# Performance work log

Measured on AMD Instinct MI355X. Metric: run time of the kernel, lower is better.

## Reference

```python
import jax, jax.numpy as jnp
import numpy as np

N, E, B = 8000, 24000, 256
ATOM, BOND, H, HEADS, L = 133, 14, 256, 8, 5
NEG, EPS = 0.2, 1e-5


def _ln(x, g, b):
    m = x.mean(-1, keepdims=True)
    v = ((x - m) ** 2).mean(-1, keepdims=True)
    return (x - m) * jax.lax.rsqrt(v + EPS) * g + b


def setup_inputs() -> dict:
    key = jax.random.key(0)
    ks = jax.random.split(key, 12)
    s = lambda k, shp, fan: (jax.random.normal(k, shp, jnp.float32) / np.float32(np.sqrt(fan)))
    inp = {
        "x": jax.random.normal(ks[0], (N, ATOM), jnp.float32),
        "edge_attr": jax.random.normal(ks[1], (E, BOND), jnp.float32),
        "emb_W": s(ks[2], (ATOM, H), ATOM), "emb_b": jnp.zeros((H,), jnp.float32),
        "emb_g": jnp.ones((H,), jnp.float32), "emb_beta": jnp.zeros((H,), jnp.float32),
        "Wl": s(ks[3], (L, H, HEADS * H), H), "Wr": s(ks[4], (L, H, HEADS * H), H),
        "We": s(ks[5], (L, BOND, HEADS * H), BOND),
        "att": s(ks[6], (L, HEADS, H), H),
        "bias": jnp.zeros((L, H), jnp.float32),
        "ln_g": jnp.ones((L, H), jnp.float32), "ln_b": jnp.zeros((L, H), jnp.float32),
        "g1W": s(ks[7], (H, H // 2), H), "g1b": jnp.zeros((H // 2,), jnp.float32),
        "g2W": s(ks[8], (H // 2, 1), H // 2), "g2b": jnp.zeros((1,), jnp.float32),
        "edge_index": jax.random.randint(ks[9], (2, E), 0, N, dtype=jnp.int32),
        "batch_vec": jnp.sort(jax.random.randint(ks[10], (N,), 0, B, dtype=jnp.int32)),
    }
    return inp


def reference(x, edge_attr, emb_W, emb_b, emb_g, emb_beta, Wl, Wr, We, att, bias,
              ln_g, ln_b, g1W, g1b, g2W, g2b, edge_index, batch_vec):
    src, dst = edge_index[0], edge_index[1]
    # GATv2Conv add_self_loops=True, fill_value='mean': self-loop edge_attr at node i
    # is the mean of edge features of edges incoming to i (zeros if none).
    deg = jax.ops.segment_sum(jnp.ones((E,), x.dtype), dst, num_segments=N)
    loop_attr = jax.ops.segment_sum(edge_attr, dst, num_segments=N) / jnp.maximum(deg, 1.0)[:, None]
    ar = jnp.arange(N)
    src_a = jnp.concatenate([src, ar])
    dst_a = jnp.concatenate([dst, ar])
    ea = jnp.concatenate([edge_attr, loop_attr], axis=0)  # [E+N, BOND]
    # atom embedding: Linear -> LayerNorm -> ReLU (dropout = identity at eval)
    h = jax.nn.relu(_ln(x @ emb_W + emb_b, emb_g, emb_beta))  # [N, H]
    for l in range(L):
        xl = (h @ Wl[l]).reshape(N, HEADS, H)  # source transform
        xr = (h @ Wr[l]).reshape(N, HEADS, H)  # destination transform
        ee = (ea @ We[l]).reshape(-1, HEADS, H)
        f = jax.nn.leaky_relu(xl[src_a] + xr[dst_a] + ee, NEG)  # [EA, HEADS, H]
        score = jnp.einsum('ehd,hd->eh', f, att[l])  # [EA, HEADS]
        # scatter-softmax over edges sharing a destination (self-loops => no empty segment)
        m = jax.ops.segment_max(score, dst_a, num_segments=N)
        ex = jnp.exp(score - m[dst_a])
        alpha = ex / jax.ops.segment_sum(ex, dst_a, num_segments=N)[dst_a]
        msg = xl[src_a] * alpha[..., None]
        out = jax.ops.segment_sum(msg, dst_a, num_segments=N).mean(axis=1) + bias[l]  # concat=False: head mean
        h = _ln(out + h, ln_g[l], ln_b[l])  # residual + LayerNorm
    # GlobalAttention readout: gate_nn -> scatter-softmax per graph -> weighted sum
    gate = jax.nn.relu(h @ g1W + g1b) @ g2W + g2b  # [N, 1]
    gm = jax.ops.segment_max(gate, batch_vec, num_segments=B)
    ge = jnp.exp(gate - gm[batch_vec])
    w = ge / jnp.maximum(jax.ops.segment_sum(ge, batch_vec, num_segments=B)[batch_vec], 1e-16)
    return jax.ops.segment_sum(w * h, batch_vec, num_segments=B)  # [B, H]
```

## Files before the change

### kernel.cpp

```cpp
#include <hip/hip_runtime.h>
#include <math.h>

#define N_NODES 8000
#define N_EDGES 24000
#define NB      256
#define ATOM    133
#define BOND    14
#define HDIM    256
#define HEADS   8
#define NLAYERS 5
#define NEG     0.2f
#define LN_EPS  1e-5f
#define HH      (HEADS * HDIM)
#define MPAD    8064
#define EA      (N_EDGES + N_NODES)

typedef __attribute__((ext_vector_type(8))) short short8;
typedef __attribute__((ext_vector_type(4))) float floatx4;
typedef __attribute__((ext_vector_type(2))) _Float16 h2_t;
typedef unsigned short ushort_t;

__device__ __forceinline__ ushort_t f2bf(float f) {
  unsigned u = __float_as_uint(f);
  unsigned r = (u + 0x7fff + ((u >> 16) & 1)) >> 16;
  return (ushort_t)r;
}
__device__ __forceinline__ float bf2f(ushort_t h) {
  return __uint_as_float(((unsigned)h) << 16);
}
__device__ __forceinline__ float4 ldbf4(const ushort_t* p) {
  ushort4 u = *(const ushort4*)p;
  return make_float4(bf2f(u.x), bf2f(u.y), bf2f(u.z), bf2f(u.w));
}

__device__ __forceinline__ h2_t u2h2(unsigned u) {
  union { unsigned u; h2_t h; } c; c.u = u; return c.h;
}
__device__ __forceinline__ unsigned f2h2(float a, float b) {
  union { h2_t h; unsigned u; } c;
  c.h.x = (_Float16)a; c.h.y = (_Float16)b;
  return c.u;
}
#if defined(__has_builtin)
#if __has_builtin(__builtin_amdgcn_fdot2)
#define FDOT2(a, b, c) __builtin_amdgcn_fdot2((a), (b), (c), false)
#endif
#endif
#ifndef FDOT2
__device__ __forceinline__ float fdot2_sw(h2_t a, h2_t b, float c) {
  return c + (float)a.x * (float)b.x + (float)a.y * (float)b.y;
}
#define FDOT2 fdot2_sw
#endif

template <int CTRL, int RMASK>
__device__ __forceinline__ float dpp_add(float x) {
  return x + __int_as_float(__builtin_amdgcn_update_dpp(
      0, __float_as_int(x), CTRL, RMASK, 0xF, true));
}
__device__ __forceinline__ float wave_sum_u(float x) {
  x = dpp_add<0xB1, 0xF>(x);
  x = dpp_add<0x4E, 0xF>(x);
  x = dpp_add<0x141, 0xF>(x);
  x = dpp_add<0x140, 0xF>(x);
  x = dpp_add<0x142, 0xA>(x);
  x = dpp_add<0x143, 0xC>(x);
  return __int_as_float(__builtin_amdgcn_readlane(__float_as_int(x), 63));
}

__device__ __forceinline__ void load_lds16(const void* g, void* l) {
  __builtin_amdgcn_global_load_lds((const __attribute__((address_space(1))) unsigned int*)g,
                                   (__attribute__((address_space(3))) unsigned int*)l,
                                   16, 0, 0);
}

__device__ __forceinline__ float block_reduce_sum(float v, float* red) {
  int t = threadIdx.x;
  red[t] = v; __syncthreads();
  for (int s = blockDim.x >> 1; s > 0; s >>= 1) {
    if (t < s) red[t] += red[t + s];
    __syncthreads();
  }
  float r = red[0]; __syncthreads();
  return r;
}
__device__ __forceinline__ float block_reduce_max(float v, float* red) {
  int t = threadIdx.x;
  red[t] = v; __syncthreads();
  for (int s = blockDim.x >> 1; s > 0; s >>= 1) {
    if (t < s) red[t] = fmaxf(red[t], red[t + s]);
    __syncthreads();
  }
  float r = red[0]; __syncthreads();
  return r;
}

__global__ void k_deg(const int* __restrict__ dst, int* __restrict__ deg) {
  int e = blockIdx.x * blockDim.x + threadIdx.x;
  if (e < N_EDGES) atomicAdd(&deg[dst[e]], 1);
}

__global__ void k_scan(const int* __restrict__ cnt, int* __restrict__ offs, int n) {
  __shared__ int wsum[8];
  __shared__ int carry_s;
  int t = threadIdx.x, w = t >> 6, lane = t & 63;
  if (t == 0) carry_s = 0;
  __syncthreads();
  for (int base = 0; base < n; base += 256) {
    int i = base + t;
    int v = (i < n) ? cnt[i] : 0;
    int x = v;
#pragma unroll
    for (int off = 1; off < 64; off <<= 1) {
      int u = __shfl_up(x, off);
      if (lane >= off) x += u;
    }
    if (lane == 63) wsum[w] = x;
    __syncthreads();
    int wpre = 0;
    for (int q = 0; q < w; q++) wpre += wsum[q];
    int carry = carry_s;
    if (i < n) offs[i] = carry + wpre + x - v;
    __syncthreads();
    if (t == 255) carry_s = carry + wpre + x;
    __syncthreads();
  }
  if (t == 0) offs[n] = carry_s;
}

__global__ void k_fill(const int* __restrict__ src, const int* __restrict__ dst,
                       const int* __restrict__ row_start, int* __restrict__ cursor,
                       int* __restrict__ csr_eid, int* __restrict__ csr_src) {
  int e = blockIdx.x * blockDim.x + threadIdx.x;
  if (e < N_EDGES) {
    int d = dst[e];
    int pos = atomicAdd(&cursor[d], 1);
    int q = row_start[d] + pos;
    csr_eid[q] = e;
    csr_src[q] = src[e];
  } else if (e < EA) {
    csr_src[e] = e - N_EDGES;
  }
}

__global__ void k_loop_attr(const float* __restrict__ edge_attr, const int* __restrict__ row_start,
                            const int* __restrict__ csr_eid, float* __restrict__ loop_attr) {
  int t = blockIdx.x * blockDim.x + threadIdx.x;
  if (t >= N_NODES * BOND) return;
  int i = t / BOND, k = t % BOND;
  int beg = row_start[i], end = row_start[i + 1];
  float s = 0.f;
  for (int p = beg; p < end; p++) s += edge_attr[(size_t)csr_eid[p] * BOND + k];
  int degv = end - beg;
  loop_attr[(size_t)i * BOND + k] = s / fmaxf((float)degv, 1.f);
}

__global__ void k_feat(const float* __restrict__ edge_attr, const float* __restrict__ loop_attr,
                       const int* __restrict__ csr_eid, unsigned* __restrict__ feat16) {
  int t = blockIdx.x * blockDim.x + threadIdx.x;
  if (t >= EA * 8) return;
  int p = t >> 3, k2 = t & 7;
  unsigned v = 0;
  if (k2 < 7) {
    const float* sp = (p < N_EDGES) ? (edge_attr + (size_t)csr_eid[p] * BOND)
                                    : (loop_attr + (size_t)(p - N_EDGES) * BOND);
    v = f2h2(sp[2 * k2], sp[2 * k2 + 1]);
  }
  feat16[(size_t)p * 8 + k2] = v;
}

__global__ __launch_bounds__(256) void k_build_bt(const float* __restrict__ Wl,
                                                  const float* __restrict__ Wr,
                                                  ushort_t* __restrict__ Bt) {
  __shared__ ushort_t s[64 * 40];
  int l = blockIdx.x >> 6;
  int n0 = (blockIdx.x & 63) * 64;
  int t = threadIdx.x;
  int nl = t & 63;
  int kr = t >> 6;
  int n = n0 + nl;
  const float* Wsrc = (n < HH) ? Wl : Wr;
  int nn = (n < HH) ? n : n - HH;
  const float* base = Wsrc + (size_t)l * HDIM * HH + nn;
  for (int kb = 0; kb < 256; kb += 32) {
#pragma unroll
    for (int q = 0; q < 8; q++) {
      int k = kb + q * 4 + kr;
      s[nl * 40 + q * 4 + kr] = f2bf(base[(size_t)k * HH]);
    }
    __syncthreads();
    {
      int n2 = t >> 2, c = t & 3;
      short8 v = *(const short8*)&s[n2 * 40 + c * 8];
      *(short8*)&Bt[((size_t)l * 4096 + n0 + n2) * 256 + kb + c * 8] = v;
    }
    __syncthreads();
  }
}

__global__ __launch_bounds__(256) void k_embed(const float* __restrict__ x, const float* __restrict__ W,
                                               const float* __restrict__ b, const float* __restrict__ g,
                                               const float* __restrict__ beta, float* __restrict__ h,
                                               ushort_t* __restrict__ Abuf) {
  __shared__ float xs[ATOM];
  __shared__ float red[256];
  int i = blockIdx.x, j = threadIdx.x;
  if (j < ATOM) xs[j] = x[(size_t)i * ATOM + j];
  __syncthreads();
  float acc = b[j];
  for (int k = 0; k < ATOM; k++) acc += xs[k] * W[(size_t)k * HDIM + j];
  float mean = block_reduce_sum(acc, red) * (1.f / HDIM);
  float diff = acc - mean;
  float var = block_reduce_sum(diff * diff, red) * (1.f / HDIM);
  float vn = diff * rsqrtf(var + LN_EPS) * g[j] + beta[j];
  float r = fmaxf(vn, 0.f);
  h[(size_t)i * HDIM + j] = r;
  Abuf[(size_t)i * 256 + j] = f2bf(r);
}

__global__ __launch_bounds__(256) void k_gemm_mfma(const ushort_t* __restrict__ A,
                                                   const ushort_t* __restrict__ Bt,
                                                   ushort_t* __restrict__ C) {
  __shared__ char smem[65536];
  ushort_t* Cs = (ushort_t*)smem;
  const int tid = threadIdx.x;
  const int wave = tid >> 6, lane = tid & 63;
  const int bm = blockIdx.y * 128, bn = blockIdx.x * 128;
  const int wm = (wave >> 1) * 64, wn = (wave & 1) * 64;

  const ushort_t* agA[4];
  const ushort_t* agB[4];
  int lofs[4];
#pragma unroll
  for (int j = 0; j < 4; j++) {
    int c = j * 256 + tid;
    int row = c >> 3, col = (c & 7) * 8;
    agA[j] = A  + (size_t)(bm + row) * 256 + col;
    agB[j] = Bt + (size_t)(bn + row) * 256 + col;
    lofs[j] = c * 8;
  }

#pragma unroll
  for (int j = 0; j < 4; j++) load_lds16(agA[j], (ushort_t*)smem + lofs[j]);
#pragma unroll
  for (int j = 0; j < 4; j++) load_lds16(agB[j], (ushort_t*)(smem + 16384) + lofs[j]);

  floatx4 acc[4][4] = {};
  const int mrow = lane & 15;
  const int kq = (lane >> 4) * 8;

  for (int s = 0; s < 4; s++) {
    __syncthreads();
    if (s < 3) {
      char* nb = smem + ((s + 1) & 1) * 32768;
      const int k0 = (s + 1) * 64;
#pragma unroll
      for (int j = 0; j < 4; j++) load_lds16(agA[j] + k0, (ushort_t*)nb + lofs[j]);
#pragma unroll
      for (int j = 0; j < 4; j++) load_lds16(agB[j] + k0, (ushort_t*)(nb + 16384) + lofs[j]);
    }
    const ushort_t* As = (const ushort_t*)(smem + (s & 1) * 32768);
    const ushort_t* Bs = As + 8192;
#pragma unroll
    for (int half = 0; half < 2; half++) {
      const int kk = half * 32 + kq;
      short8 af[4], bfr[4];
#pragma unroll
      for (int mi = 0; mi < 4; mi++)
        af[mi] = *(const short8*)&As[(wm + mi * 16 + mrow) * 64 + kk];
#pragma unroll
      for (int ni = 0; ni < 4; ni++)
        bfr[ni] = *(const short8*)&Bs[(wn + ni * 16 + mrow) * 64 + kk];
#pragma unroll
      for (int mi = 0; mi < 4; mi++)
#pragma unroll
        for (int ni = 0; ni < 4; ni++)
          acc[mi][ni] = __builtin_amdgcn_mfma_f32_16x16x32_bf16(af[mi], bfr[ni], acc[mi][ni], 0, 0, 0);
    }
  }
  __syncthreads();
  const int lr = (lane >> 4) * 4, lc = lane & 15;
#pragma unroll
  for (int mi = 0; mi < 4; mi++)
#pragma unroll
    for (int ni = 0; ni < 4; ni++)
#pragma unroll
      for (int r = 0; r < 4; r++)
        Cs[(wm + mi * 16 + lr + r) * 136 + wn + ni * 16 + lc] = f2bf(acc[mi][ni][r]);
  __syncthreads();
#pragma unroll
  for (int it = 0; it < 8; it++) {
    int idx = it * 256 + tid;
    int row = idx >> 4, chunk = idx & 15;
    int grow = bm + row;
    if (grow < N_NODES) {
      short8 v = *(const short8*)&Cs[row * 136 + chunk * 8];
      *(short8*)&C[(size_t)grow * 4096 + bn + chunk * 8] = v;
    }
  }
}

__device__ __forceinline__ float score_f16(const float4& xl, const float4& xr,
                                           const uint4& cfa, const uint4& cfb,
                                           const unsigned w2[7][4], const float4& at4) {
  float e0 = 0.f, e1 = 0.f, e2 = 0.f, e3 = 0.f;
  unsigned cf[7] = {cfa.x, cfa.y, cfa.z, cfa.w, cfb.x, cfb.y, cfb.z};
#pragma unroll
  for (int k2 = 0; k2 < 7; k2++) {
    h2_t f = u2h2(cf[k2]);
    e0 = FDOT2(f, u2h2(w2[k2][0]), e0);
    e1 = FDOT2(f, u2h2(w2[k2][1]), e1);
    e2 = FDOT2(f, u2h2(w2[k2][2]), e2);
    e3 = FDOT2(f, u2h2(w2[k2][3]), e3);
  }
  float f0 = xl.x + xr.x + e0; f0 = f0 > 0.f ? f0 : NEG * f0;
  float f1 = xl.y + xr.y + e1; f1 = f1 > 0.f ? f1 : NEG * f1;
  float f2 = xl.z + xr.z + e2; f2 = f2 > 0.f ? f2 : NEG * f2;
  float f3 = xl.w + xr.w + e3; f3 = f3 > 0.f ? f3 : NEG * f3;
  float sp = f0 * at4.x + f1 * at4.y + f2 * at4.z + f3 * at4.w;
  return wave_sum_u(sp);
}

__global__ __launch_bounds__(512) void k_attn(const ushort_t* __restrict__ xlr,
    const unsigned* __restrict__ feat16,
    const float* __restrict__ We, const float* __restrict__ att,
    const int* __restrict__ row_start, const int* __restrict__ csr_src,
    const float* __restrict__ bias, const float* __restrict__ lng,
    const float* __restrict__ lnb,
    float* __restrict__ h, ushort_t* __restrict__ Abuf) {
  __shared__ ushort_t sacc[2][HEADS][264];
  const int tid = threadIdx.x, hh = tid >> 6, lane = tid & 63;
  unsigned w2[7][4];
#pragma unroll
  for (int k2 = 0; k2 < 7; k2++) {
    float4 a = *(const float4*)&We[(size_t)(2 * k2) * HH + hh * HDIM + lane * 4];
    float4 b = *(const float4*)&We[(size_t)(2 * k2 + 1) * HH + hh * HDIM + lane * 4];
    w2[k2][0] = f2h2(a.x, b.x); w2[k2][1] = f2h2(a.y, b.y);
    w2[k2][2] = f2h2(a.z, b.z); w2[k2][3] = f2h2(a.w, b.w);
  }
  float4 at4 = *(const float4*)&att[hh * HDIM + lane * 4];
  const int node0 = blockIdx.x * 2;

#pragma unroll
  for (int ni = 0; ni < 2; ni++) {
    int i = node0 + ni;
    int beg = row_start[i], end = row_start[i + 1];
    float4 xr4 = ldbf4(&xlr[(size_t)i * 4096 + 2048 + hh * HDIM + lane * 4]);
    float4 xl4 = ldbf4(&xlr[(size_t)i * 4096 + hh * HDIM + lane * 4]);
    int pself = N_EDGES + i;
    uint4 fa = *(const uint4*)&feat16[(size_t)pself * 8];
    uint4 fb = *(const uint4*)&feat16[(size_t)pself * 8 + 4];
    float4 px4;
    uint4 pfa, pfb;
    if (beg < end) {
      int sn0 = __builtin_amdgcn_readfirstlane(csr_src[beg]);
      px4 = ldbf4(&xlr[(size_t)sn0 * 4096 + hh * HDIM + lane * 4]);
      pfa = *(const uint4*)&feat16[(size_t)beg * 8];
      pfb = *(const uint4*)&feat16[(size_t)beg * 8 + 4];
    }
    float s = score_f16(xl4, xr4, fa, fb, w2, at4);
    float m = s, l = 1.f;
    float o0 = xl4.x, o1 = xl4.y, o2 = xl4.z, o3 = xl4.w;
    for (int p = beg; p < end; p++) {
      float4 x4 = px4;
      uint4 cfa = pfa, cfb = pfb;
      if (p + 1 < end) {
        int sn = __builtin_amdgcn_readfirstlane(csr_src[p + 1]);
        px4 = ldbf4(&xlr[(size_t)sn * 4096 + hh * HDIM + lane * 4]);
        pfa = *(const uint4*)&feat16[(size_t)(p + 1) * 8];
        pfb = *(const uint4*)&feat16[(size_t)(p + 1) * 8 + 4];
      }
      float s2 = score_f16(x4, xr4, cfa, cfb, w2, at4);
      if (s2 > m) {
        float c = __expf(m - s2);
        o0 = o0 * c + x4.x; o1 = o1 * c + x4.y;
        o2 = o2 * c + x4.z; o3 = o3 * c + x4.w;
        l = l * c + 1.f;
        m = s2;
      } else {
        float wv = __expf(s2 - m);
        o0 += wv * x4.x; o1 += wv * x4.y;
        o2 += wv * x4.z; o3 += wv * x4.w;
        l += wv;
      }
    }
    float inv = 1.f / l;
    ushort4 st;
    st.x = f2bf(o0 * inv); st.y = f2bf(o1 * inv);
    st.z = f2bf(o2 * inv); st.w = f2bf(o3 * inv);
    *(ushort4*)&sacc[ni][hh][lane * 4] = st;
  }
  __syncthreads();
  if (hh < 2) {
    int i = node0 + hh;
    float4 hres = *(const float4*)&h[(size_t)i * HDIM + lane * 4];
    float hr[4] = {hres.x, hres.y, hres.z, hres.w};
    float v[4] = {0.f, 0.f, 0.f, 0.f};
#pragma unroll
    for (int q = 0; q < HEADS; q++) {
      ushort4 u = *(const ushort4*)&sacc[hh][q][lane * 4];
      v[0] += bf2f(u.x); v[1] += bf2f(u.y); v[2] += bf2f(u.z); v[3] += bf2f(u.w);
    }
    float4 bias4 = *(const float4*)&bias[lane * 4];
    float bi[4] = {bias4.x, bias4.y, bias4.z, bias4.w};
#pragma unroll
    for (int j = 0; j < 4; j++) v[j] = v[j] * 0.125f + bi[j] + hr[j];
    float mean = wave_sum_u(v[0] + v[1] + v[2] + v[3]) * (1.f / HDIM);
    float df[4], vr = 0.f;
#pragma unroll
    for (int j = 0; j < 4; j++) { df[j] = v[j] - mean; vr += df[j] * df[j]; }
    float rstd = rsqrtf(wave_sum_u(vr) * (1.f / HDIM) + LN_EPS);
    float4 g4 = *(const float4*)&lng[lane * 4];
    float4 b4 = *(const float4*)&lnb[lane * 4];
    float gg[4] = {g4.x, g4.y, g4.z, g4.w};
    float bb[4] = {b4.x, b4.y, b4.z, b4.w};
    float r[4];
    ushort4 hi;
#pragma unroll
    for (int j = 0; j < 4; j++) r[j] = df[j] * rstd * gg[j] + bb[j];
    hi.x = f2bf(r[0]); hi.y = f2bf(r[1]); hi.z = f2bf(r[2]); hi.w = f2bf(r[3]);
    *(float4*)&h[(size_t)i * HDIM + lane * 4] = make_float4(r[0], r[1], r[2], r[3]);
    *(ushort4*)&Abuf[(size_t)i * 256 + lane * 4] = hi;
  }
}

__global__ __launch_bounds__(128) void k_gate(const float* __restrict__ h, const float* __restrict__ g1W,
                                              const float* __restrict__ g1b, const float* __restrict__ g2W,
                                              const float* __restrict__ g2b, float* __restrict__ gate) {
  __shared__ float hs[4][HDIM];
  __shared__ float red[4][132];
  const int j = threadIdx.x;
  const int i0 = blockIdx.x * 4;
#pragma unroll
  for (int it = 0; it < 2; it++) {
    int c = it * 128 + j;
    int node = c >> 6, off = (c & 63) * 4;
    *(float4*)&hs[node][off] = *(const float4*)&h[(size_t)(i0 + node) * HDIM + off];
  }
  __syncthreads();
  float acc[4];
  float b = g1b[j];
#pragma unroll
  for (int n = 0; n < 4; n++) acc[n] = b;
  for (int k = 0; k < HDIM; k++) {
    float w = g1W[(size_t)k * (HDIM / 2) + j];
#pragma unroll
    for (int n = 0; n < 4; n++) acc[n] += hs[n][k] * w;
  }
  float w2 = g2W[j];
#pragma unroll
  for (int n = 0; n < 4; n++) red[n][j] = fmaxf(acc[n], 0.f) * w2;
  __syncthreads();
  int n = j >> 5, l2 = j & 31;
  float s = red[n][l2] + red[n][l2 + 32] + red[n][l2 + 64] + red[n][l2 + 96];
#pragma unroll
  for (int off = 16; off > 0; off >>= 1) s += __shfl_xor(s, off, 32);
  if (l2 == 0) gate[i0 + n] = s + g2b[0];
}

__global__ void k_gcount(const int* __restrict__ batch, int* __restrict__ gcnt) {
  int i = blockIdx.x * blockDim.x + threadIdx.x;
  if (i < N_NODES) atomicAdd(&gcnt[batch[i]], 1);
}

__global__ __launch_bounds__(256) void k_readout(const float* __restrict__ h, const float* __restrict__ gate,
                                                 const int* __restrict__ goff, float* __restrict__ out) {
  __shared__ float red[256];
  int b = blockIdx.x, t = threadIdx.x;
  int beg = goff[b], end = goff[b + 1];
  if (end <= beg) { out[(size_t)b * HDIM + t] = 0.f; return; }
  float lm = -3.4e38f;
  for (int i = beg + t; i < end; i += 256) lm = fmaxf(lm, gate[i]);
  float m = block_reduce_max(lm, red);
  float ls = 0.f;
  for (int i = beg + t; i < end; i += 256) ls += __expf(gate[i] - m);
  float s = block_reduce_sum(ls, red);
  float inv = 1.f / fmaxf(s, 1e-16f);
  float acc = 0.f;
  for (int i = beg; i < end; i++) acc += __expf(gate[i] - m) * h[(size_t)i * HDIM + t];
  out[(size_t)b * HDIM + t] = acc * inv;
}

extern "C" void kernel_launch(void* const* d_in, const int* in_sizes, int n_in,
                              void* d_out, int out_size, void* d_ws, size_t ws_size,
                              hipStream_t stream) {
  const float* x         = (const float*)d_in[0];
  const float* edge_attr = (const float*)d_in[1];
  const float* emb_W     = (const float*)d_in[2];
  const float* emb_b     = (const float*)d_in[3];
  const float* emb_g     = (const float*)d_in[4];
  const float* emb_beta  = (const float*)d_in[5];
  const float* Wl        = (const float*)d_in[6];
  const float* Wr        = (const float*)d_in[7];
  const float* We        = (const float*)d_in[8];
  const float* att       = (const float*)d_in[9];
  const float* bias      = (const float*)d_in[10];
  const float* ln_g      = (const float*)d_in[11];
  const float* ln_b      = (const float*)d_in[12];
  const float* g1W       = (const float*)d_in[13];
  const float* g1b       = (const float*)d_in[14];
  const float* g2W       = (const float*)d_in[15];
  const float* g2b       = (const float*)d_in[16];
  const int*   edge_index= (const int*)d_in[17];
  const int*   batch     = (const int*)d_in[18];
  float* out = (float*)d_out;

  const int* src = edge_index;
  const int* dst = edge_index + N_EDGES;

  char* p = (char*)d_ws;
  auto alloc = [&](size_t bytes) -> void* {
    void* r = (void*)p;
    p += (bytes + 255) & ~(size_t)255;
    return r;
  };
  int*   deg       = (int*)alloc((size_t)N_NODES * 4);
  int*   row_start = (int*)alloc((size_t)(N_NODES + 1) * 4);
  int*   cursor    = (int*)alloc((size_t)N_NODES * 4);
  int*   csr_eid   = (int*)alloc((size_t)N_EDGES * 4);
  int*   csr_src   = (int*)alloc((size_t)EA * 4);
  float* loop_attr = (float*)alloc((size_t)N_NODES * BOND * 4);
  unsigned* feat16 = (unsigned*)alloc((size_t)EA * 8 * 4);
  float* h         = (float*)alloc((size_t)N_NODES * HDIM * 4);
  ushort_t* Abuf   = (ushort_t*)alloc((size_t)MPAD * 256 * 2);
  ushort_t* Bt     = (ushort_t*)alloc((size_t)NLAYERS * 4096 * 256 * 2);
  ushort_t* xlr    = (ushort_t*)alloc((size_t)N_NODES * 4096 * 2);
  float* gate      = (float*)alloc((size_t)N_NODES * 4);
  int*   gcnt      = (int*)alloc((size_t)NB * 4);
  int*   goff      = (int*)alloc((size_t)(NB + 1) * 4);

  hipMemsetAsync(deg, 0, (size_t)N_NODES * 4, stream);
  hipMemsetAsync(cursor, 0, (size_t)N_NODES * 4, stream);
  hipMemsetAsync(gcnt, 0, (size_t)NB * 4, stream);

  k_deg<<<(N_EDGES + 255) / 256, 256, 0, stream>>>(dst, deg);
  k_scan<<<1, 256, 0, stream>>>(deg, row_start, N_NODES);
  k_fill<<<(EA + 255) / 256, 256, 0, stream>>>(src, dst, row_start, cursor,
                                               csr_eid, csr_src);
  k_loop_attr<<<(N_NODES * BOND + 255) / 256, 256, 0, stream>>>(edge_attr, row_start, csr_eid, loop_attr);
  k_feat<<<(EA * 8 + 255) / 256, 256, 0, stream>>>(edge_attr, loop_attr, csr_eid, feat16);
  k_build_bt<<<NLAYERS * 64, 256, 0, stream>>>(Wl, Wr, Bt);
  k_embed<<<N_NODES, 256, 0, stream>>>(x, emb_W, emb_b, emb_g, emb_beta, h, Abuf);

  dim3 ggrid(4096 / 128, MPAD / 128);
  for (int l = 0; l < NLAYERS; l++) {
    const ushort_t* Bt_l = Bt + (size_t)l * 4096 * 256;
    const float* We_l  = We + (size_t)l * BOND * HH;
    const float* att_l = att + (size_t)l * HEADS * HDIM;
    k_gemm_mfma<<<ggrid, 256, 0, stream>>>(Abuf, Bt_l, xlr);
    k_attn<<<N_NODES / 2, 512, 0, stream>>>(xlr, feat16, We_l, att_l,
                                            row_start, csr_src,
                                            bias + (size_t)l * HDIM, ln_g + (size_t)l * HDIM,
                                            ln_b + (size_t)l * HDIM, h, Abuf);
  }

  k_gate<<<N_NODES / 4, 128, 0, stream>>>(h, g1W, g1b, g2W, g2b, gate);
  k_gcount<<<(N_NODES + 255) / 256, 256, 0, stream>>>(batch, gcnt);
  k_scan<<<1, 256, 0, stream>>>(gcnt, goff, NB);
  k_readout<<<NB, 256, 0, stream>>>(h, gate, goff, out);
}
```

Measured before the change: 717.7 us.

## Interleave two destination nodes' edge loops and halve GEMM K-tile to cut LDS

The attention aggregation kernel now walks the incoming-edge lists of its two destination nodes together in one loop instead of one after the other. This gives two independent gather and score chains per iteration so memory latency can overlap. Separately, the MFMA GEMM switches from a K-tile of 64 to 32, reducing shared memory from 64KB to about 34KB to allow more resident blocks. The costs are twice as many barriers and pipeline stages in the GEMM, and higher register pressure plus wasted score work on the shorter edge list.

Result: slower. 752.3 us (+4.8%).

```diff
diff --git a/kernel.cpp b/kernel.cpp
--- a/kernel.cpp
+++ b/kernel.cpp
@@ -221,62 +221,58 @@
 __global__ __launch_bounds__(256) void k_gemm_mfma(const ushort_t* __restrict__ A,
                                                    const ushort_t* __restrict__ Bt,
                                                    ushort_t* __restrict__ C) {
-  __shared__ char smem[65536];
+  __shared__ char smem[34816];
   ushort_t* Cs = (ushort_t*)smem;
   const int tid = threadIdx.x;
   const int wave = tid >> 6, lane = tid & 63;
   const int bm = blockIdx.y * 128, bn = blockIdx.x * 128;
   const int wm = (wave >> 1) * 64, wn = (wave & 1) * 64;
 
-  const ushort_t* agA[4];
-  const ushort_t* agB[4];
-  int lofs[4];
-#pragma unroll
-  for (int j = 0; j < 4; j++) {
+  const ushort_t* agA[2];
+  const ushort_t* agB[2];
+  int lofs[2];
+#pragma unroll
+  for (int j = 0; j < 2; j++) {
     int c = j * 256 + tid;
-    int row = c >> 3, col = (c & 7) * 8;
+    int row = c >> 2, col = (c & 3) * 8;
     agA[j] = A  + (size_t)(bm + row) * 256 + col;
     agB[j] = Bt + (size_t)(bn + row) * 256 + col;
     lofs[j] = c * 8;
   }
 
 #pragma unroll
-  for (int j = 0; j < 4; j++) load_lds16(agA[j], (ushort_t*)smem + lofs[j]);
-#pragma unroll
-  for (int j = 0; j < 4; j++) load_lds16(agB[j], (ushort_t*)(smem + 16384) + lofs[j]);
+  for (int j = 0; j < 2; j++) load_lds16(agA[j], (ushort_t*)smem + lofs[j]);
+#pragma unroll
+  for (int j = 0; j < 2; j++) load_lds16(agB[j], (ushort_t*)(smem + 8192) + lofs[j]);
 
   floatx4 acc[4][4] = {};
   const int mrow = lane & 15;
   const int kq = (lane >> 4) * 8;
 
-  for (int s = 0; s < 4; s++) {
-    __syncthreads();
-    if (s < 3) {
-      char* nb = smem + ((s + 1) & 1) * 32768;
-      const int k0 = (s + 1) * 64;
-#pragma unroll
-      for (int j = 0; j < 4; j++) load_lds16(agA[j] + k0, (ushort_t*)nb + lofs[j]);
-#pragma unroll
-      for (int j = 0; j < 4; j++) load_lds16(agB[j] + k0, (ushort_t*)(nb + 16384) + lofs[j]);
-    }
-    const ushort_t* As = (const ushort_t*)(smem + (s & 1) * 32768);
-    const ushort_t* Bs = As + 8192;
-#pragma unroll
-    for (int half = 0; half < 2; half++) {
-      const int kk = half * 32 + kq;
-      short8 af[4], bfr[4];
-#pragma unroll
-      for (int mi = 0; mi < 4; mi++)
-        af[mi] = *(const short8*)&As[(wm + mi * 16 + mrow) * 64 + kk];
+  for (int s = 0; s < 8; s++) {
+    __syncthreads();
+    if (s < 7) {
+      char* nb = smem + ((s + 1) & 1) * 16384;
+      const int k0 = (s + 1) * 32;
+#pragma unroll
+      for (int j = 0; j < 2; j++) load_lds16(agA[j] + k0, (ushort_t*)nb + lofs[j]);
+#pragma unroll
+      for (int j = 0; j < 2; j++) load_lds16(agB[j] + k0, (ushort_t*)(nb + 8192) + lofs[j]);
+    }
+    const ushort_t* As = (const ushort_t*)(smem + (s & 1) * 16384);
+    const ushort_t* Bs = As + 4096;
+    short8 af[4], bfr[4];
+#pragma unroll
+    for (int mi = 0; mi < 4; mi++)
+      af[mi] = *(const short8*)&As[(wm + mi * 16 + mrow) * 32 + kq];
+#pragma unroll
+    for (int ni = 0; ni < 4; ni++)
+      bfr[ni] = *(const short8*)&Bs[(wn + ni * 16 + mrow) * 32 + kq];
+#pragma unroll
+    for (int mi = 0; mi < 4; mi++)
 #pragma unroll
       for (int ni = 0; ni < 4; ni++)
-        bfr[ni] = *(const short8*)&Bs[(wn + ni * 16 + mrow) * 64 + kk];
-#pragma unroll
-      for (int mi = 0; mi < 4; mi++)
-#pragma unroll
-        for (int ni = 0; ni < 4; ni++)
-          acc[mi][ni] = __builtin_amdgcn_mfma_f32_16x16x32_bf16(af[mi], bfr[ni], acc[mi][ni], 0, 0, 0);
-    }
+        acc[mi][ni] = __builtin_amdgcn_mfma_f32_16x16x32_bf16(af[mi], bfr[ni], acc[mi][ni], 0, 0, 0);
   }
   __syncthreads();
   const int lr = (lane >> 4) * 4, lc = lane & 15;
@@ -340,55 +336,98 @@
   }
   float4 at4 = *(const float4*)&att[hh * HDIM + lane * 4];
   const int node0 = blockIdx.x * 2;
-
-#pragma unroll
-  for (int ni = 0; ni < 2; ni++) {
-    int i = node0 + ni;
-    int beg = row_start[i], end = row_start[i + 1];
-    float4 xr4 = ldbf4(&xlr[(size_t)i * 4096 + 2048 + hh * HDIM + lane * 4]);
-    float4 xl4 = ldbf4(&xlr[(size_t)i * 4096 + hh * HDIM + lane * 4]);
-    int pself = N_EDGES + i;
-    uint4 fa = *(const uint4*)&feat16[(size_t)pself * 8];
-    uint4 fb = *(const uint4*)&feat16[(size_t)pself * 8 + 4];
-    float4 px4;
-    uint4 pfa, pfb;
-    if (beg < end) {
-      int sn0 = __builtin_amdgcn_readfirstlane(csr_src[beg]);
-      px4 = ldbf4(&xlr[(size_t)sn0 * 4096 + hh * HDIM + lane * 4]);
-      pfa = *(const uint4*)&feat16[(size_t)beg * 8];
-      pfb = *(const uint4*)&feat16[(size_t)beg * 8 + 4];
-    }
-    float s = score_f16(xl4, xr4, fa, fb, w2, at4);
-    float m = s, l = 1.f;
-    float o0 = xl4.x, o1 = xl4.y, o2 = xl4.z, o3 = xl4.w;
-    for (int p = beg; p < end; p++) {
-      float4 x4 = px4;
-      uint4 cfa = pfa, cfb = pfb;
-      if (p + 1 < end) {
-        int sn = __builtin_amdgcn_readfirstlane(csr_src[p + 1]);
-        px4 = ldbf4(&xlr[(size_t)sn * 4096 + hh * HDIM + lane * 4]);
-        pfa = *(const uint4*)&feat16[(size_t)(p + 1) * 8];
-        pfb = *(const uint4*)&feat16[(size_t)(p + 1) * 8 + 4];
+  const int iA = node0, iB = node0 + 1;
+  const int begA = row_start[iA], endA = row_start[iA + 1];
+  const int begB = endA, endB = row_start[iB + 1];
+  const int lenA = endA - begA, lenB = endB - begB;
+
+  float4 xrA = ldbf4(&xlr[(size_t)iA * 4096 + 2048 + hh * HDIM + lane * 4]);
+  float4 xrB = ldbf4(&xlr[(size_t)iB * 4096 + 2048 + hh * HDIM + lane * 4]);
+  float4 xlA = ldbf4(&xlr[(size_t)iA * 4096 + hh * HDIM + lane * 4]);
+  float4 xlB = ldbf4(&xlr[(size_t)iB * 4096 + hh * HDIM + lane * 4]);
+  uint4 faA = *(const uint4*)&feat16[(size_t)(N_EDGES + iA) * 8];
+  uint4 fbA = *(const uint4*)&feat16[(size_t)(N_EDGES + iA) * 8 + 4];
+  uint4 faB = *(const uint4*)&feat16[(size_t)(N_EDGES + iB) * 8];
+  uint4 fbB = *(const uint4*)&feat16[(size_t)(N_EDGES + iB) * 8 + 4];
+
+  float4 pxA = xlA, pxB = xlB;
+  uint4 pfaA = faA, pfbA = fbA, pfaB = faB, pfbB = fbB;
+  if (lenA > 0) {
+    int sn = __builtin_amdgcn_readfirstlane(csr_src[begA]);
+    pxA = ldbf4(&xlr[(size_t)sn * 4096 + hh * HDIM + lane * 4]);
+    pfaA = *(const uint4*)&feat16[(size_t)begA * 8];
+    pfbA = *(const uint4*)&feat16[(size_t)begA * 8 + 4];
+  }
+  if (lenB > 0) {
+    int sn = __builtin_amdgcn_readfirstlane(csr_src[begB]);
+    pxB = ldbf4(&xlr[(size_t)sn * 4096 + hh * HDIM + lane * 4]);
+    pfaB = *(const uint4*)&feat16[(size_t)begB * 8];
+    pfbB = *(const uint4*)&feat16[(size_t)begB * 8 + 4];
+  }
+
+  float mA = score_f16(xlA, xrA, faA, fbA, w2, at4);
+  float mB = score_f16(xlB, xrB, faB, fbB, w2, at4);
+  float lA = 1.f, lB = 1.f;
+  float oA0 = xlA.x, oA1 = xlA.y, oA2 = xlA.z, oA3 = xlA.w;
+  float oB0 = xlB.x, oB1 = xlB.y, oB2 = xlB.z, oB3 = xlB.w;
+
+  const int len = max(lenA, lenB);
+  for (int t = 0; t < len; t++) {
+    bool doA = t < lenA, doB = t < lenB;
+    float4 xA = pxA, xB = pxB;
+    uint4 cfaA = pfaA, cfbA = pfbA, cfaB = pfaB, cfbB = pfbB;
+    if (t + 1 < lenA) {
+      int sn = __builtin_amdgcn_readfirstlane(csr_src[begA + t + 1]);
+      pxA = ldbf4(&xlr[(size_t)sn * 4096 + hh * HDIM + lane * 4]);
+      pfaA = *(const uint4*)&feat16[(size_t)(begA + t + 1) * 8];
+      pfbA = *(const uint4*)&feat16[(size_t)(begA + t + 1) * 8 + 4];
+    }
+    if (t + 1 < lenB) {
+      int sn = __builtin_amdgcn_readfirstlane(csr_src[begB + t + 1]);
+      pxB = ldbf4(&xlr[(size_t)sn * 4096 + hh * HDIM + lane * 4]);
+      pfaB = *(const uint4*)&feat16[(size_t)(begB + t + 1) * 8];
+      pfbB = *(const uint4*)&feat16[(size_t)(begB + t + 1) * 8 + 4];
+    }
+    float s2A = score_f16(xA, xrA, cfaA, cfbA, w2, at4);
+    float s2B = score_f16(xB, xrB, cfaB, cfbB, w2, at4);
+    if (doA) {
+      if (s2A > mA) {
+        float c = __expf(mA - s2A);
+        oA0 = oA0 * c + xA.x; oA1 = oA1 * c + xA.y;
+        oA2 = oA2 * c + xA.z; oA3 = oA3 * c + xA.w;
+        lA = lA * c + 1.f;
+        mA = s2A;
+      } else {
+        float wv = __expf(s2A - mA);
+        oA0 += wv * xA.x; oA1 += wv * xA.y;
+        oA2 += wv * xA.z; oA3 += wv * xA.w;
+        lA += wv;
       }
-      float s2 = score_f16(x4, xr4, cfa, cfb, w2, at4);
-      if (s2 > m) {
-        float c = __expf(m - s2);
-        o0 = o0 * c + x4.x; o1 = o1 * c + x4.y;
-        o2 = o2 * c + x4.z; o3 = o3 * c + x4.w;
-        l = l * c + 1.f;
-        m = s2;
+    }
+    if (doB) {
+      if (s2B > mB) {
+        float c = __expf(mB - s2B);
+        oB0 = oB0 * c + xB.x; oB1 = oB1 * c + xB.y;
+        oB2 = oB2 * c + xB.z; oB3 = oB3 * c + xB.w;
+        lB = lB * c + 1.f;
+        mB = s2B;
       } else {
-        float wv = __expf(s2 - m);
-        o0 += wv * x4.x; o1 += wv * x4.y;
-        o2 += wv * x4.z; o3 += wv * x4.w;
-        l += wv;
+        float wv = __expf(s2B - mB);
+        oB0 += wv * xB.x; oB1 += wv * xB.y;
+        oB2 += wv * xB.z; oB3 += wv * xB.w;
+        lB += wv;
       }
     }
-    float inv = 1.f / l;
-    ushort4 st;
-    st.x = f2bf(o0 * inv); st.y = f2bf(o1 * inv);
-    st.z = f2bf(o2 * inv); st.w = f2bf(o3 * inv);
-    *(ushort4*)&sacc[ni][hh][lane * 4] = st;
+  }
+  {
+    float invA = 1.f / lA, invB = 1.f / lB;
+    ushort4 stA, stB;
+    stA.x = f2bf(oA0 * invA); stA.y = f2bf(oA1 * invA);
+    stA.z = f2bf(oA2 * invA); stA.w = f2bf(oA3 * invA);
+    stB.x = f2bf(oB0 * invB); stB.y = f2bf(oB1 * invB);
+    stB.z = f2bf(oB2 * invB); stB.w = f2bf(oB3 * invB);
+    *(ushort4*)&sacc[0][hh][lane * 4] = stA;
+    *(ushort4*)&sacc[1][hh][lane * 4] = stB;
   }
   __syncthreads();
   if (hh < 2) {
```
